# Optimization experiments

Measured on AMD Instinct MI355X. Metric: run time of the kernel, lower is better.

Reference implementation:

```python
import jax, jax.numpy as jnp
import numpy as np

N = 50000        # nodes
E = 800000       # edges (avg degree 16)
F_IN = 128
H = 128
C = 16


def setup_inputs() -> dict:
    key = jax.random.key(0)
    ks = jax.random.split(key, 12)
    x = jax.random.normal(ks[0], (N, F_IN), dtype=jnp.float32)
    edges = jax.random.randint(ks[1], (2, E), 0, N, dtype=jnp.int32)
    dims = [(F_IN, H), (H, H // 2), (H // 2, H // 4), (H // 4, H // 8), (H // 8, C)]
    params = {}
    for i, (di, do) in enumerate(dims):
        params[f"W{i+1}"] = jax.random.normal(ks[2 + 2 * i], (di, do), dtype=jnp.float32) * (1.0 / np.sqrt(di)).astype(np.float32)
        params[f"b{i+1}"] = jax.random.normal(ks[3 + 2 * i], (do,), dtype=jnp.float32) * 0.01
    return {"x": x, "edges": edges, **params}


def reference(x, edges, W1, b1, W2, b2, W3, b3, W4, b4, W5, b5):
    src, dst = edges[0], edges[1]
    ones = jnp.ones((E,), x.dtype)
    # symmetric ('both') normalization with degree clamped to >= 1 (DGL GraphConv default)
    out_deg = jnp.clip(jax.ops.segment_sum(ones, src, num_segments=N), 1.0, None)
    in_deg = jnp.clip(jax.ops.segment_sum(ones, dst, num_segments=N), 1.0, None)
    norm_src = (out_deg ** -0.5)[:, None]   # [N,1]
    norm_dst = (in_deg ** -0.5)[:, None]    # [N,1]

    def graph_conv(h, W, b):
        h = h @ W                                  # dense transform first (out <= in)
        msgs = (h * norm_src)[src]                 # [E, d_out] gather
        agg = jax.ops.segment_sum(msgs, dst, num_segments=N)  # scatter-add SpMM
        return agg * norm_dst + b

    h = x
    for W, b in ((W1, b1), (W2, b2), (W3, b3), (W4, b4), (W5, b5)):
        h = jax.nn.relu(graph_conv(h, W, b))
    return h
```

## Files before the change

### kernel.cpp

```cpp
#include <hip/hip_runtime.h>
#include <hip/hip_bf16.h>


#define THREADS 256
#define HIST_B 128
#define HWORDS 12500
#define RS_BLOCKS 196
#define G1BLKS 782
#define C4 (HIST_B / 4)

typedef __attribute__((ext_vector_type(8))) short short8_t;
typedef __attribute__((ext_vector_type(4))) float float4_t;

__device__ __forceinline__ unsigned short f2bf_rne(float f) {
    unsigned u = __builtin_bit_cast(unsigned, f);
    unsigned r = u + 0x7fffu + ((u >> 16) & 1u);
    return (unsigned short)(r >> 16);
}
__device__ __forceinline__ float bf2f(unsigned short h) {
    return __builtin_bit_cast(float, ((unsigned)h) << 16);
}

template<int NT, bool NORM, bool ASCALE>
__device__ __forceinline__ void quant_epilogue(float4_t* acc, const float* __restrict__ norm,
                                               const float* __restrict__ ascale,
                                               short* __restrict__ outq, float* __restrict__ qscale,
                                               int M, int blk, int tid,
                                               int ostride, int ocol0, int qstride, int qoff) {
    const int w    = tid >> 6;
    const int lane = tid & 63;
    const int ln   = lane & 15;
    const int quad = lane >> 4;
    const int orow = blk * 64 + w * 16 + quad * 4;
#pragma unroll
    for (int i = 0; i < 4; ++i) {
        int r = orow + i;
        float m = 0.f;
#pragma unroll
        for (int nt = 0; nt < NT; ++nt) m = fmaxf(m, fabsf(acc[nt][i]));
#pragma unroll
        for (int off = 1; off < 16; off <<= 1) m = fmaxf(m, __shfl_xor(m, off));
        float s = 1.f;
        if (NORM) s = (r < M) ? norm[r] : 0.f;
        if (ASCALE && r < M) s *= ascale[r];
        float rowmax = m * s;
        float inv = (rowmax > 0.f) ? (32767.f / rowmax) : 0.f;
        if (r < M) {
            if (ln == 0) qscale[r * qstride + qoff] = rowmax * (1.f / 32767.f);
#pragma unroll
            for (int nt = 0; nt < NT; ++nt)
                outq[(size_t)r * ostride + ocol0 + nt * 16 + ln] =
                    (short)(int)__builtin_rintf(acc[nt][i] * s * inv);
        }
    }
}

template<int K, int NOUT>
__device__ __forceinline__ void gemm_core_q(const short* __restrict__ Aq,
                                            const float* __restrict__ ascale,
                                            const short* lh, const short* ll,
                                            const float* __restrict__ norm,
                                            short* __restrict__ outq, float* __restrict__ qscale,
                                            int M, int blk, int tid) {
    constexpr int Kp  = (K + 31) & ~31;
    constexpr int STR = Kp + 8;
    constexpr int NT  = NOUT / 16;
    const int w    = tid >> 6;
    const int lane = tid & 63;
    const int ln   = lane & 15;
    const int quad = lane >> 4;
    const int row  = blk * 64 + w * 16 + ln;
    const bool rv  = row < M;

    float4_t acc[NT];
#pragma unroll
    for (int i = 0; i < NT; ++i) acc[i] = (float4_t){0.f, 0.f, 0.f, 0.f};

#pragma unroll
    for (int kt = 0; kt < Kp / 32; ++kt) {
        const int k0 = kt * 32 + quad * 8;
        short8_t qv = (short8_t)(short)0;
        if (rv && k0 < K) qv = *(const short8_t*)&Aq[(size_t)row * K + k0];
        short8_t ahi, alo;
#pragma unroll
        for (int j = 0; j < 8; ++j) {
            float a = (float)qv[j];
            unsigned short h = f2bf_rne(a);
            ahi[j] = (short)h;
            alo[j] = (short)f2bf_rne(a - bf2f(h));
        }
#pragma unroll
        for (int nt = 0; nt < NT; ++nt) {
            const int bidx = (nt * 16 + ln) * STR + kt * 32 + quad * 8;
            short8_t bh = *(const short8_t*)&lh[bidx];
            short8_t bl = *(const short8_t*)&ll[bidx];
            acc[nt] = __builtin_amdgcn_mfma_f32_16x16x32_bf16(ahi, bh, acc[nt], 0, 0, 0);
            acc[nt] = __builtin_amdgcn_mfma_f32_16x16x32_bf16(ahi, bl, acc[nt], 0, 0, 0);
            acc[nt] = __builtin_amdgcn_mfma_f32_16x16x32_bf16(alo, bh, acc[nt], 0, 0, 0);
        }
    }
    quant_epilogue<NT, true, true>(acc, norm, ascale, outq, qscale, M, blk, tid,
                                   NOUT, 0, 1, 0);
}

template<int K, int NOUT, int DINP>
__device__ __forceinline__ void gemm_core_lds(const float* As,
                                              const short* lh, const short* ll,
                                              const float* __restrict__ norm,
                                              short* __restrict__ outq, float* __restrict__ qscale,
                                              int M, int blk, int tid) {
    constexpr int Kp  = (K + 31) & ~31;
    constexpr int STR = Kp + 8;
    constexpr int NT  = NOUT / 16;
    const int w    = tid >> 6;
    const int lane = tid & 63;
    const int ln   = lane & 15;
    const int quad = lane >> 4;
    const int rloc = w * 16 + ln;
    const bool rv  = (blk * 64 + rloc) < M;

    float4_t acc[NT];
#pragma unroll
    for (int i = 0; i < NT; ++i) acc[i] = (float4_t){0.f, 0.f, 0.f, 0.f};

#pragma unroll
    for (int kt = 0; kt < Kp / 32; ++kt) {
        const int k0 = kt * 32 + quad * 8;
        float a[8];
        if (rv && k0 < K) {
            float4 v0 = *(const float4*)&As[rloc * DINP + k0];
            float4 v1 = *(const float4*)&As[rloc * DINP + k0 + 4];
            a[0] = v0.x; a[1] = v0.y; a[2] = v0.z; a[3] = v0.w;
            a[4] = v1.x; a[5] = v1.y; a[6] = v1.z; a[7] = v1.w;
        } else {
#pragma unroll
            for (int j = 0; j < 8; ++j) a[j] = 0.f;
        }
        short8_t ahi, alo;
#pragma unroll
        for (int j = 0; j < 8; ++j) {
            unsigned short h = f2bf_rne(a[j]);
            ahi[j] = (short)h;
            alo[j] = (short)f2bf_rne(a[j] - bf2f(h));
        }
#pragma unroll
        for (int nt = 0; nt < NT; ++nt) {
            const int bidx = (nt * 16 + ln) * STR + kt * 32 + quad * 8;
            short8_t bh = *(const short8_t*)&lh[bidx];
            short8_t bl = *(const short8_t*)&ll[bidx];
            acc[nt] = __builtin_amdgcn_mfma_f32_16x16x32_bf16(ahi, bh, acc[nt], 0, 0, 0);
            acc[nt] = __builtin_amdgcn_mfma_f32_16x16x32_bf16(ahi, bl, acc[nt], 0, 0, 0);
            acc[nt] = __builtin_amdgcn_mfma_f32_16x16x32_bf16(alo, bh, acc[nt], 0, 0, 0);
        }
    }
    quant_epilogue<NT, true, false>(acc, norm, nullptr, outq, qscale, M, blk, tid,
                                    NOUT, 0, 1, 0);
}

__device__ __forceinline__ void conv_one(const float* __restrict__ W, short* __restrict__ hi,
                                         short* __restrict__ lo, int K, int NOUT, int STR, int i) {
    int n = i / STR;
    int kk = i % STR;
    float v = (kk < K) ? W[(size_t)kk * NOUT + n] : 0.f;
    unsigned short h = f2bf_rne(v);
    hi[i] = (short)h;
    lo[i] = (short)f2bf_rne(v - bf2f(h));
}

__global__ __launch_bounds__(THREADS)
void packed0_kernel(const float* __restrict__ x, const float* __restrict__ W1,
                    const float* __restrict__ W2, const float* __restrict__ W3,
                    const float* __restrict__ W4, const float* __restrict__ W5,
                    short* __restrict__ tq, float* __restrict__ qscale2,
                    const int* __restrict__ src, const int* __restrict__ dst,
                    unsigned* __restrict__ p_src, unsigned* __restrict__ p_dst,
                    unsigned char* __restrict__ rank, int* __restrict__ flags,
                    short* w2h, short* w2l, short* w3h, short* w3l,
                    short* w4h, short* w4l, short* w5h, short* w5l,
                    int E, int chunk, int N) {
    __shared__ __align__(16) char smem[50048];
    const int blk = blockIdx.x;
    const int t = threadIdx.x;

    if (blk < G1BLKS) {
        short* lh = (short*)smem;
        short* ll = (short*)smem + 8704;

        const int lane = t & 63;
        const int ln   = lane & 15;
        const int quad = lane >> 4;
        const int row  = blk * 64 + (t >> 6) * 16 + ln;
        const bool rv  = row < N;

        short8_t ahi[4], alo[4];
#pragma unroll
        for (int kt = 0; kt < 4; ++kt) {
            const int k0 = kt * 32 + quad * 8;
            float a[8];
            if (rv) {
                float4 v0 = *(const float4*)&x[(size_t)row * 128 + k0];
                float4 v1 = *(const float4*)&x[(size_t)row * 128 + k0 + 4];
                a[0] = v0.x; a[1] = v0.y; a[2] = v0.z; a[3] = v0.w;
                a[4] = v1.x; a[5] = v1.y; a[6] = v1.z; a[7] = v1.w;
            } else {
#pragma unroll
                for (int j = 0; j < 8; ++j) a[j] = 0.f;
            }
#pragma unroll
            for (int j = 0; j < 8; ++j) {
                unsigned short h = f2bf_rne(a[j]);
                ahi[kt][j] = (short)h;
                alo[kt][j] = (short)f2bf_rne(a[j] - bf2f(h));
            }
        }

        for (int h = 0; h < 2; ++h) {
            for (int j = t; j < 128 * 64; j += THREADS) {
                int kk = j >> 6, n = j & 63;
                float v = W1[kk * 128 + h * 64 + n];
                unsigned short hh = f2bf_rne(v);
                lh[n * 136 + kk] = (short)hh;
                ll[n * 136 + kk] = (short)f2bf_rne(v - bf2f(hh));
            }
            __syncthreads();

            float4_t acc[4];
#pragma unroll
            for (int i = 0; i < 4; ++i) acc[i] = (float4_t){0.f, 0.f, 0.f, 0.f};
#pragma unroll
            for (int kt = 0; kt < 4; ++kt) {
#pragma unroll
                for (int nt = 0; nt < 4; ++nt) {
                    const int bidx = (nt * 16 + ln) * 136 + kt * 32 + quad * 8;
                    short8_t bh = *(const short8_t*)&lh[bidx];
                    short8_t bl = *(const short8_t*)&ll[bidx];
                    acc[nt] = __builtin_amdgcn_mfma_f32_16x16x32_bf16(ahi[kt], bh, acc[nt], 0, 0, 0);
                    acc[nt] = __builtin_amdgcn_mfma_f32_16x16x32_bf16(ahi[kt], bl, acc[nt], 0, 0, 0);
                    acc[nt] = __builtin_amdgcn_mfma_f32_16x16x32_bf16(alo[kt], bh, acc[nt], 0, 0, 0);
                }
            }
            quant_epilogue<4, false, false>(acc, nullptr, nullptr, tq, qscale2, N, blk, t,
                                            128, h * 64, 2, h);
            if (h == 0) __syncthreads();
        }
    } else if (blk < G1BLKS + 2 * HIST_B) {
        unsigned* bins = (unsigned*)smem;
        const int hb = blk - G1BLKS;
        const bool is_dst = hb < HIST_B;
        const int b = is_dst ? hb : hb - HIST_B;
        const int e0 = b * chunk;
        int e1 = e0 + chunk; if (e1 > E) e1 = E;
        const int* __restrict__ idx = is_dst ? dst : src;
        unsigned* __restrict__ pout = is_dst ? p_dst : p_src;

        for (int w = t; w < HWORDS; w += THREADS) bins[w] = 0;
        __syncthreads();
        for (int e = e0 + t; e < e1; e += THREADS) {
            int d = idx[e];
            unsigned sh = (unsigned)(d & 3) * 8u;
            unsigned old = atomicAdd(&bins[d >> 2], 1u << sh);
            if (is_dst) rank[e] = (unsigned char)((old >> sh) & 0xffu);
        }
        __syncthreads();
        for (int w = t; w < HWORDS; w += THREADS)
            pout[(size_t)b * HWORDS + w] = bins[w];
    } else {
        int cb = blk - G1BLKS - 2 * HIST_B;
        if (cb == 48) {
            flags[t] = 0;
            return;
        }
        int i = cb * THREADS + t;
        if (i < 8704)                        conv_one(W2, w2h, w2l, 128, 64, 136, i);
        else if ((i -= 8704) < 2304)         conv_one(W3, w3h, w3l, 64, 32, 72, i);
        else if ((i -= 2304) < 640)          conv_one(W4, w4h, w4l, 32, 16, 40, i);
        else { i -= 640;                     conv_one(W5, w5h, w5l, 16, 16, 40, i); }
    }
}

__global__ __launch_bounds__(THREADS)
void reduce_scan_kernel(const unsigned* __restrict__ p_src, unsigned* __restrict__ p_dst,
                        float* __restrict__ norm_src, float* __restrict__ norm_dst,
                        float* __restrict__ qscale2, int* __restrict__ row_ptr,
                        int* __restrict__ flags, int N) {
    __shared__ unsigned qd[4][64];
    __shared__ unsigned qs[4][64];
    __shared__ int sscan[64];
    __shared__ int bexcl_sh;
    const int t  = threadIdx.x;
    const int b  = blockIdx.x;
    const int q  = t >> 6;
    const int wl = t & 63;
    const int w  = b * 64 + wl;
    const bool wv = (w < HWORDS);

    unsigned vals[C4];
    unsigned dsum = 0, ssum = 0;
    if (wv) {
#pragma unroll
        for (int i = 0; i < C4; ++i) {
            int c = q * C4 + i;
            vals[i] = p_dst[(size_t)c * HWORDS + w];
            dsum += vals[i];
        }
#pragma unroll
        for (int i = 0; i < C4; ++i) {
            int c = q * C4 + i;
            ssum += p_src[(size_t)c * HWORDS + w];
        }
    }
    qd[q][wl] = dsum;
    qs[q][wl] = ssum;
    __syncthreads();

    unsigned off = 0, dfull = 0, sfull = 0;
#pragma unroll
    for (int qq = 0; qq < 4; ++qq) {
        unsigned v = qd[qq][wl];
        if (qq < q) off += v;
        dfull += v;
        sfull += qs[qq][wl];
    }

    if (wv) {
        unsigned run = off;
#pragma unroll
        for (int i = 0; i < C4; ++i) {
            int c = q * C4 + i;
            p_dst[(size_t)c * HWORDS + w] = run;
            run += vals[i];
        }
    }

    int d0 = 0, d1 = 0, d2 = 0, d3 = 0, wdeg = 0;
    if (q == 0) {
        d0 = (int)(dfull & 0xffu); d1 = (int)((dfull >> 8) & 0xffu);
        d2 = (int)((dfull >> 16) & 0xffu); d3 = (int)(dfull >> 24);
        wdeg = d0 + d1 + d2 + d3;
        if (wv) {
#pragma unroll
            for (int l = 0; l < 4; ++l) {
                int node = 4 * w + l;
                int dd = (l == 0) ? d0 : (l == 1) ? d1 : (l == 2) ? d2 : d3;
                int ds = (int)((sfull >> (8 * l)) & 0xffu);
                norm_dst[node] = rsqrtf((float)(dd < 1 ? 1 : dd));
                float ns = rsqrtf((float)(ds < 1 ? 1 : ds));
                norm_src[node] = ns;
                qscale2[2 * node]     *= ns;
                qscale2[2 * node + 1] *= ns;
            }
        }
        sscan[wl] = wv ? wdeg : 0;
    }
    __syncthreads();
    for (int o = 1; o < 64; o <<= 1) {
        int u = 0;
        if (t < 64 && t >= o) u = sscan[t - o];
        __syncthreads();
        if (t < 64) sscan[t] += u;
        __syncthreads();
    }
    const int btotal = sscan[63];

    if (t == 0) atomicExch(&flags[b], btotal + 1);
    if (t < 64) {
        int v = 0;
        for (int p = t; p < b; p += 64) {
            int f;
            do { f = atomicAdd(&flags[p], 0); } while (f == 0);
            v += f - 1;
        }
#pragma unroll
        for (int o = 1; o < 64; o <<= 1) v += __shfl_xor(v, o);
        if (t == 0) bexcl_sh = v;
    }
    __syncthreads();

    if (q == 0 && wv) {
        int pre = bexcl_sh + sscan[wl] - wdeg;
        int n0 = 4 * w;
        row_ptr[n0 + 0] = pre; pre += d0;
        row_ptr[n0 + 1] = pre; pre += d1;
        row_ptr[n0 + 2] = pre; pre += d2;
        row_ptr[n0 + 3] = pre;
    }
    if (b == RS_BLOCKS - 1 && t == 0) row_ptr[N] = bexcl_sh + btotal;
}

__global__ __launch_bounds__(THREADS)
void scatter_kernel(const int* __restrict__ src, const int* __restrict__ dst,
                    const unsigned char* __restrict__ rank,
                    const int* __restrict__ row_ptr, const unsigned* __restrict__ p_dst,
                    int* __restrict__ col, int E, int chunk) {
    const int bc  = blockIdx.x >> 2;
    const int sub = blockIdx.x & 3;
    const int qch = (chunk + 3) >> 2;
    const int e0 = bc * chunk;
    int e1 = e0 + chunk; if (e1 > E) e1 = E;
    int s = e0 + sub * qch;
    int send = s + qch; if (send > e1) send = e1;
    for (int e = s + threadIdx.x; e < send; e += THREADS) {
        int d = dst[e];
        unsigned sh = (unsigned)(d & 3) * 8u;
        unsigned pre = (p_dst[(size_t)bc * HWORDS + (d >> 2)] >> sh) & 0xffu;
        col[row_ptr[d] + (int)pre + (int)rank[e]] = src[e];
    }
}

__global__ __launch_bounds__(THREADS)
void agg1_q_kernel(const short* __restrict__ tq, const float* __restrict__ qscale2,
                   const int* __restrict__ row_ptr, const int* __restrict__ col,
                   const float* __restrict__ norm_dst, const float* __restrict__ bias,
                   short* __restrict__ outq, float* __restrict__ qs_out, int N) {
    const int tid  = threadIdx.x;
    const int ln   = tid & 15;
    const int ep   = (tid >> 4) & 3;
    const int g    = tid >> 6;
    const int node = blockIdx.x * 4 + g;
    if (node >= N) return;

    const int half = ln >> 3;
    const int beg = row_ptr[node];
    const int end = row_ptr[node + 1];

    float acc[8];
#pragma unroll
    for (int c = 0; c < 8; ++c) acc[c] = 0.f;

    int j = beg + ep;
    for (; j + 4 < end; j += 8) {
        int s0 = col[j];
        int s1 = col[j + 4];
        short8_t v0 = *(const short8_t*)&tq[(size_t)s0 * 128 + ln * 8];
        short8_t v1 = *(const short8_t*)&tq[(size_t)s1 * 128 + ln * 8];
        float c0 = qscale2[2 * s0 + half];
        float c1 = qscale2[2 * s1 + half];
#pragma unroll
        for (int c = 0; c < 8; ++c)
            acc[c] += (float)v0[c] * c0 + (float)v1[c] * c1;
    }
    if (j < end) {
        int s0 = col[j];
        short8_t v0 = *(const short8_t*)&tq[(size_t)s0 * 128 + ln * 8];
        float c0 = qscale2[2 * s0 + half];
#pragma unroll
        for (int c = 0; c < 8; ++c) acc[c] += (float)v0[c] * c0;
    }

#pragma unroll
    for (int c = 0; c < 8; ++c) {
        acc[c] += __shfl_xor(acc[c], 16);
        acc[c] += __shfl_xor(acc[c], 32);
    }

    float nd = norm_dst[node];
    float vals[8];
    float m = 0.f;
#pragma unroll
    for (int c = 0; c < 8; ++c) {
        vals[c] = fmaxf(acc[c] * nd + bias[ln * 8 + c], 0.f);
        m = fmaxf(m, vals[c]);
    }
#pragma unroll
    for (int off = 1; off < 16; off <<= 1) m = fmaxf(m, __shfl_xor(m, off));
    float inv = (m > 0.f) ? (32767.f / m) : 0.f;

    if (ep == 0) {
        short8_t q;
#pragma unroll
        for (int c = 0; c < 8; ++c) q[c] = (short)(int)__builtin_rintf(vals[c] * inv);
        *(short8_t*)&outq[(size_t)node * 128 + ln * 8] = q;
        if (ln == 0) qs_out[node] = m * (1.f / 32767.f);
    }
}

template<int K, int NOUT>
__global__ __launch_bounds__(THREADS)
void gemm_mfma_q_kernel(const short* __restrict__ Aq, const float* __restrict__ ascale,
                        const short* __restrict__ wt_hi, const short* __restrict__ wt_lo,
                        const float* __restrict__ norm,
                        short* __restrict__ outq, float* __restrict__ qscale, int M) {
    constexpr int Kp  = (K + 31) & ~31;
    constexpr int STR = Kp + 8;

    __shared__ short lh[NOUT * STR];
    __shared__ short ll[NOUT * STR];

    const int tid = threadIdx.x;
    {
        constexpr int CNT = NOUT * STR / 2;
        const int* gh = (const int*)wt_hi;
        const int* gl = (const int*)wt_lo;
        int* sh = (int*)lh;
        int* sl = (int*)ll;
        for (int i = tid; i < CNT; i += THREADS) { sh[i] = gh[i]; sl[i] = gl[i]; }
    }
    __syncthreads();
    gemm_core_q<K, NOUT>(Aq, ascale, lh, ll, norm, outq, qscale, M, blockIdx.x, tid);
}

template<int D>
__global__ __launch_bounds__(THREADS)
void agg_q_kernel(const short* __restrict__ tq, const float* __restrict__ qscale,
                  const int* __restrict__ row_ptr, const int* __restrict__ col,
                  const float* __restrict__ norm_dst, const float* __restrict__ bias,
                  float* __restrict__ out, int N) {
    constexpr int TPN = D / 8;
    constexpr int NPB = THREADS / TPN;
    const int tid  = threadIdx.x;
    const int ln   = tid % TPN;
    const int g    = tid / TPN;
    const int node = blockIdx.x * NPB + g;
    if (node >= N) return;

    const int beg = row_ptr[node];
    const int end = row_ptr[node + 1];

    float acc[8];
#pragma unroll
    for (int c = 0; c < 8; ++c) acc[c] = 0.f;

    int j = beg;
    for (; j + 3 < end; j += 4) {
        int s0 = col[j], s1 = col[j + 1], s2 = col[j + 2], s3 = col[j + 3];
        short8_t v0 = *(const short8_t*)&tq[(size_t)s0 * D + ln * 8];
        short8_t v1 = *(const short8_t*)&tq[(size_t)s1 * D + ln * 8];
        short8_t v2 = *(const short8_t*)&tq[(size_t)s2 * D + ln * 8];
        short8_t v3 = *(const short8_t*)&tq[(size_t)s3 * D + ln * 8];
        float c0 = qscale[s0], c1 = qscale[s1], c2 = qscale[s2], c3 = qscale[s3];
#pragma unroll
        for (int c = 0; c < 8; ++c)
            acc[c] += (float)v0[c] * c0 + (float)v1[c] * c1
                    + (float)v2[c] * c2 + (float)v3[c] * c3;
    }
    for (; j < end; ++j) {
        int s0 = col[j];
        short8_t v0 = *(const short8_t*)&tq[(size_t)s0 * D + ln * 8];
        float c0 = qscale[s0];
#pragma unroll
        for (int c = 0; c < 8; ++c) acc[c] += (float)v0[c] * c0;
    }

    float nd = norm_dst[node];
    float4 b0 = *(const float4*)&bias[ln * 8];
    float4 b1 = *(const float4*)&bias[ln * 8 + 4];
    float4 o0, o1;
    o0.x = fmaxf(acc[0] * nd + b0.x, 0.f);
    o0.y = fmaxf(acc[1] * nd + b0.y, 0.f);
    o0.z = fmaxf(acc[2] * nd + b0.z, 0.f);
    o0.w = fmaxf(acc[3] * nd + b0.w, 0.f);
    o1.x = fmaxf(acc[4] * nd + b1.x, 0.f);
    o1.y = fmaxf(acc[5] * nd + b1.y, 0.f);
    o1.z = fmaxf(acc[6] * nd + b1.z, 0.f);
    o1.w = fmaxf(acc[7] * nd + b1.w, 0.f);
    *(float4*)&out[(size_t)node * D + ln * 8] = o0;
    *(float4*)&out[(size_t)node * D + ln * 8 + 4] = o1;
}

template<int DIN, int NOUT>
__global__ __launch_bounds__(THREADS)
void fused_agg_gemm_kernel(const short* __restrict__ tq_in, const float* __restrict__ qs_in,
                           const int* __restrict__ row_ptr, const int* __restrict__ col,
                           const float* __restrict__ norm_dst, const float* __restrict__ bias,
                           const short* __restrict__ wt_hi, const short* __restrict__ wt_lo,
                           const float* __restrict__ norm_src,
                           short* __restrict__ tq_out, float* __restrict__ qs_out, int N) {
    constexpr int Kp   = (DIN + 31) & ~31;
    constexpr int STR  = Kp + 8;
    constexpr int DINP = DIN + 4;
    constexpr int TPN  = DIN / 8;

    __shared__ float As[64 * DINP];
    __shared__ short lh[NOUT * STR];
    __shared__ short ll[NOUT * STR];

    const int tid = threadIdx.x;
    {
        constexpr int CNT = NOUT * STR / 2;
        const int* gh = (const int*)wt_hi;
        const int* gl = (const int*)wt_lo;
        int* sh = (int*)lh;
        int* sl = (int*)ll;
        for (int i = tid; i < CNT; i += THREADS) { sh[i] = gh[i]; sl[i] = gl[i]; }
    }

    const int ln = tid % TPN;
    for (int n0 = tid / TPN; n0 < 64; n0 += THREADS / TPN) {
        const int node = blockIdx.x * 64 + n0;
        if (node < N) {
            const int beg = row_ptr[node];
            const int end = row_ptr[node + 1];
            float acc[8];
#pragma unroll
            for (int c = 0; c < 8; ++c) acc[c] = 0.f;
            int j = beg;
            for (; j + 3 < end; j += 4) {
                int s0 = col[j], s1 = col[j + 1], s2 = col[j + 2], s3 = col[j + 3];
                short8_t v0 = *(const short8_t*)&tq_in[(size_t)s0 * DIN + ln * 8];
                short8_t v1 = *(const short8_t*)&tq_in[(size_t)s1 * DIN + ln * 8];
                short8_t v2 = *(const short8_t*)&tq_in[(size_t)s2 * DIN + ln * 8];
                short8_t v3 = *(const short8_t*)&tq_in[(size_t)s3 * DIN + ln * 8];
                float c0 = qs_in[s0], c1 = qs_in[s1], c2 = qs_in[s2], c3 = qs_in[s3];
#pragma unroll
                for (int c = 0; c < 8; ++c)
                    acc[c] += (float)v0[c] * c0 + (float)v1[c] * c1
                            + (float)v2[c] * c2 + (float)v3[c] * c3;
            }
            for (; j < end; ++j) {
                int s0 = col[j];
                short8_t v0 = *(const short8_t*)&tq_in[(size_t)s0 * DIN + ln * 8];
                float c0 = qs_in[s0];
#pragma unroll
                for (int c = 0; c < 8; ++c) acc[c] += (float)v0[c] * c0;
            }
            float nd = norm_dst[node];
#pragma unroll
            for (int c = 0; c < 8; ++c)
                As[n0 * DINP + ln * 8 + c] = fmaxf(acc[c] * nd + bias[ln * 8 + c], 0.f);
        }
    }
    __syncthreads();

    gemm_core_lds<DIN, NOUT, DINP>(As, lh, ll, norm_src, tq_out, qs_out, N, blockIdx.x, tid);
}

extern "C" void kernel_launch(void* const* d_in, const int* in_sizes, int n_in,
                              void* d_out, int out_size, void* d_ws, size_t ws_size,
                              hipStream_t stream) {
    const float* x     = (const float*)d_in[0];
    const int*   edges = (const int*)d_in[1];
    const float* W1 = (const float*)d_in[2];  const float* b1 = (const float*)d_in[3];
    const float* W2 = (const float*)d_in[4];  const float* b2 = (const float*)d_in[5];
    const float* W3 = (const float*)d_in[6];  const float* b3 = (const float*)d_in[7];
    const float* W4 = (const float*)d_in[8];  const float* b4 = (const float*)d_in[9];
    const float* W5 = (const float*)d_in[10]; const float* b5 = (const float*)d_in[11];

    const int N = in_sizes[0] / 128;
    const int E = in_sizes[1] / 2;
    const int* src = edges;
    const int* dst = edges + E;

    char* ws = (char*)d_ws;
    size_t off = 0;
    auto carve = [&](size_t bytes) -> void* {
        void* p = ws + off;
        off += (bytes + 255) & ~(size_t)255;
        return p;
    };
    short* tqA      = (short*)carve((size_t)N * 128 * 2);
    short* tqB      = (short*)carve((size_t)N * 64 * 2);
    short* tqH      = (short*)carve((size_t)N * 128 * 2);
    float* norm_src = (float*)carve((size_t)N * 4);
    float* norm_dst = (float*)carve((size_t)N * 4);
    int*   row_ptr  = (int*)carve((size_t)(N + 1) * 4);
    int*   col      = (int*)carve((size_t)E * 4);
    float* qsA      = (float*)carve((size_t)2 * N * 4);
    float* qsB      = (float*)carve((size_t)N * 4);
    float* qsH      = (float*)carve((size_t)N * 4);
    int*   flags    = (int*)carve((size_t)256 * 4);
    short* wts      = (short*)carve((size_t)24576 * 2);
    unsigned* p_src = (unsigned*)carve((size_t)HIST_B * HWORDS * 4);
    unsigned* p_dst = (unsigned*)carve((size_t)HIST_B * HWORDS * 4);
    unsigned char* rank = (unsigned char*)carve((size_t)E);
    (void)ws_size;

    short* w2h = wts;            short* w2l = w2h + 8704;
    short* w3h = w2l + 8704;     short* w3l = w3h + 2304;
    short* w4h = w3l + 2304;     short* w4l = w4h + 640;
    short* w5h = w4l + 640;      short* w5l = w5h + 640;

    const int chunk = (E + HIST_B - 1) / HIST_B;
    const int gridG = (N + 63) / 64;

    packed0_kernel<<<G1BLKS + 2 * HIST_B + 49, THREADS, 0, stream>>>(
        x, W1, W2, W3, W4, W5, tqA, qsA, src, dst, p_src, p_dst, rank, flags,
        w2h, w2l, w3h, w3l, w4h, w4l, w5h, w5l, E, chunk, N);

    reduce_scan_kernel<<<RS_BLOCKS, THREADS, 0, stream>>>(
        p_src, p_dst, norm_src, norm_dst, qsA, row_ptr, flags, N);

    scatter_kernel<<<4 * HIST_B, THREADS, 0, stream>>>(src, dst, rank, row_ptr, p_dst, col, E, chunk);

    agg1_q_kernel<<<(N + 3) / 4, THREADS, 0, stream>>>(
        tqA, qsA, row_ptr, col, norm_dst, b1, tqH, qsH, N);

    gemm_mfma_q_kernel<128, 64><<<gridG, THREADS, 0, stream>>>(
        tqH, qsH, w2h, w2l, norm_src, tqA, qsA, N);

    fused_agg_gemm_kernel<64, 32><<<gridG, THREADS, 0, stream>>>(
        tqA, qsA, row_ptr, col, norm_dst, b2, w3h, w3l, norm_src, tqB, qsB, N);
    fused_agg_gemm_kernel<32, 16><<<gridG, THREADS, 0, stream>>>(
        tqB, qsB, row_ptr, col, norm_dst, b3, w4h, w4l, norm_src, tqA, qsA, N);
    fused_agg_gemm_kernel<16, 16><<<gridG, THREADS, 0, stream>>>(
        tqA, qsA, row_ptr, col, norm_dst, b4, w5h, w5l, norm_src, tqB, qsB, N);

    agg_q_kernel<16><<<(N + 127) / 128, THREADS, 0, stream>>>(
        tqB, qsB, row_ptr, col, norm_dst, b5, (float*)d_out, N);
}
```

Before: 260.0 us.

## Halve shared memory in fused first kernel via quarter-tiles and two-pass histograms

Cuts the packed0 kernel's shared-memory footprint from about 50KB to about 25KB so more blocks can be resident per CU. The first GEMM now processes W1 in four 32-column tiles instead of two 64-column tiles, which means four quantization scales per node instead of two, and the aggregation and scan kernels are updated to match. The degree histogram blocks now make two passes over their edge chunk, each covering half of the node range. The cost is twice the edge index reads and more block barriers in the histogram blocks, plus extra W1 staging rounds and scale traffic in the GEMM blocks.

```diff
diff --git a/kernel.cpp b/kernel.cpp
--- a/kernel.cpp
+++ b/kernel.cpp
@@ -5,6 +5,8 @@
 #define THREADS 256
 #define HIST_B 128
 #define HWORDS 12500
+#define HWORDS2 6250
+#define NPR 25000
 #define RS_BLOCKS 196
 #define G1BLKS 782
 #define C4 (HIST_B / 4)
@@ -171,20 +173,20 @@
 void packed0_kernel(const float* __restrict__ x, const float* __restrict__ W1,
                     const float* __restrict__ W2, const float* __restrict__ W3,
                     const float* __restrict__ W4, const float* __restrict__ W5,
-                    short* __restrict__ tq, float* __restrict__ qscale2,
+                    short* __restrict__ tq, float* __restrict__ qscale4,
                     const int* __restrict__ src, const int* __restrict__ dst,
                     unsigned* __restrict__ p_src, unsigned* __restrict__ p_dst,
                     unsigned char* __restrict__ rank, int* __restrict__ flags,
                     short* w2h, short* w2l, short* w3h, short* w3l,
                     short* w4h, short* w4l, short* w5h, short* w5l,
                     int E, int chunk, int N) {
-    __shared__ __align__(16) char smem[50048];
+    __shared__ __align__(16) char smem[25088];
     const int blk = blockIdx.x;
     const int t = threadIdx.x;
 
     if (blk < G1BLKS) {
         short* lh = (short*)smem;
-        short* ll = (short*)smem + 8704;
+        short* ll = (short*)smem + 4352;
 
         const int lane = t & 63;
         const int ln   = lane & 15;
@@ -214,23 +216,23 @@
             }
         }
 
-        for (int h = 0; h < 2; ++h) {
-            for (int j = t; j < 128 * 64; j += THREADS) {
-                int kk = j >> 6, n = j & 63;
-                float v = W1[kk * 128 + h * 64 + n];
+        for (int qt = 0; qt < 4; ++qt) {
+            for (int j = t; j < 128 * 32; j += THREADS) {
+                int kk = j >> 5, n = j & 31;
+                float v = W1[kk * 128 + qt * 32 + n];
                 unsigned short hh = f2bf_rne(v);
                 lh[n * 136 + kk] = (short)hh;
                 ll[n * 136 + kk] = (short)f2bf_rne(v - bf2f(hh));
             }
             __syncthreads();
 
-            float4_t acc[4];
-#pragma unroll
-            for (int i = 0; i < 4; ++i) acc[i] = (float4_t){0.f, 0.f, 0.f, 0.f};
+            float4_t acc[2];
+            acc[0] = (float4_t){0.f, 0.f, 0.f, 0.f};
+            acc[1] = (float4_t){0.f, 0.f, 0.f, 0.f};
 #pragma unroll
             for (int kt = 0; kt < 4; ++kt) {
 #pragma unroll
-                for (int nt = 0; nt < 4; ++nt) {
+                for (int nt = 0; nt < 2; ++nt) {
                     const int bidx = (nt * 16 + ln) * 136 + kt * 32 + quad * 8;
                     short8_t bh = *(const short8_t*)&lh[bidx];
                     short8_t bl = *(const short8_t*)&ll[bidx];
@@ -239,9 +241,9 @@
                     acc[nt] = __builtin_amdgcn_mfma_f32_16x16x32_bf16(alo[kt], bh, acc[nt], 0, 0, 0);
                 }
             }
-            quant_epilogue<4, false, false>(acc, nullptr, nullptr, tq, qscale2, N, blk, t,
-                                            128, h * 64, 2, h);
-            if (h == 0) __syncthreads();
+            quant_epilogue<2, false, false>(acc, nullptr, nullptr, tq, qscale4, N, blk, t,
+                                            128, qt * 32, 4, qt);
+            if (qt < 3) __syncthreads();
         }
     } else if (blk < G1BLKS + 2 * HIST_B) {
         unsigned* bins = (unsigned*)smem;
@@ -253,17 +255,24 @@
         const int* __restrict__ idx = is_dst ? dst : src;
         unsigned* __restrict__ pout = is_dst ? p_dst : p_src;
 
-        for (int w = t; w < HWORDS; w += THREADS) bins[w] = 0;
-        __syncthreads();
-        for (int e = e0 + t; e < e1; e += THREADS) {
-            int d = idx[e];
-            unsigned sh = (unsigned)(d & 3) * 8u;
-            unsigned old = atomicAdd(&bins[d >> 2], 1u << sh);
-            if (is_dst) rank[e] = (unsigned char)((old >> sh) & 0xffu);
-        }
-        __syncthreads();
-        for (int w = t; w < HWORDS; w += THREADS)
-            pout[(size_t)b * HWORDS + w] = bins[w];
+        for (int r = 0; r < 2; ++r) {
+            const int lo = r * NPR;
+            for (int w = t; w < HWORDS2; w += THREADS) bins[w] = 0;
+            __syncthreads();
+            for (int e = e0 + t; e < e1; e += THREADS) {
+                int d = idx[e];
+                int dl = d - lo;
+                if ((unsigned)dl < (unsigned)NPR) {
+                    unsigned sh = (unsigned)(dl & 3) * 8u;
+                    unsigned old = atomicAdd(&bins[dl >> 2], 1u << sh);
+                    if (is_dst) rank[e] = (unsigned char)((old >> sh) & 0xffu);
+                }
+            }
+            __syncthreads();
+            for (int w = t; w < HWORDS2; w += THREADS)
+                pout[(size_t)b * HWORDS + r * HWORDS2 + w] = bins[w];
+            if (r == 0) __syncthreads();
+        }
     } else {
         int cb = blk - G1BLKS - 2 * HIST_B;
         if (cb == 48) {
@@ -281,7 +290,7 @@
 __global__ __launch_bounds__(THREADS)
 void reduce_scan_kernel(const unsigned* __restrict__ p_src, unsigned* __restrict__ p_dst,
                         float* __restrict__ norm_src, float* __restrict__ norm_dst,
-                        float* __restrict__ qscale2, int* __restrict__ row_ptr,
+                        float* __restrict__ qscale4, int* __restrict__ row_ptr,
                         int* __restrict__ flags, int N) {
     __shared__ unsigned qd[4][64];
     __shared__ unsigned qs[4][64];
@@ -346,8 +355,10 @@
                 norm_dst[node] = rsqrtf((float)(dd < 1 ? 1 : dd));
                 float ns = rsqrtf((float)(ds < 1 ? 1 : ds));
                 norm_src[node] = ns;
-                qscale2[2 * node]     *= ns;
-                qscale2[2 * node + 1] *= ns;
+                qscale4[4 * node]     *= ns;
+                qscale4[4 * node + 1] *= ns;
+                qscale4[4 * node + 2] *= ns;
+                qscale4[4 * node + 3] *= ns;
             }
         }
         sscan[wl] = wv ? wdeg : 0;
@@ -408,7 +419,7 @@
 }
 
 __global__ __launch_bounds__(THREADS)
-void agg1_q_kernel(const short* __restrict__ tq, const float* __restrict__ qscale2,
+void agg1_q_kernel(const short* __restrict__ tq, const float* __restrict__ qscale4,
                    const int* __restrict__ row_ptr, const int* __restrict__ col,
                    const float* __restrict__ norm_dst, const float* __restrict__ bias,
                    short* __restrict__ outq, float* __restrict__ qs_out, int N) {
@@ -419,7 +430,7 @@
     const int node = blockIdx.x * 4 + g;
     if (node >= N) return;
 
-    const int half = ln >> 3;
+    const int qtr = ln >> 2;
     const int beg = row_ptr[node];
     const int end = row_ptr[node + 1];
 
@@ -433,8 +444,8 @@
         int s1 = col[j + 4];
         short8_t v0 = *(const short8_t*)&tq[(size_t)s0 * 128 + ln * 8];
         short8_t v1 = *(const short8_t*)&tq[(size_t)s1 * 128 + ln * 8];
-        float c0 = qscale2[2 * s0 + half];
-        float c1 = qscale2[2 * s1 + half];
+        float c0 = qscale4[4 * s0 + qtr];
+        float c1 = qscale4[4 * s1 + qtr];
 #pragma unroll
         for (int c = 0; c < 8; ++c)
             acc[c] += (float)v0[c] * c0 + (float)v1[c] * c1;
@@ -442,7 +453,7 @@
     if (j < end) {
         int s0 = col[j];
         short8_t v0 = *(const short8_t*)&tq[(size_t)s0 * 128 + ln * 8];
-        float c0 = qscale2[2 * s0 + half];
+        float c0 = qscale4[4 * s0 + qtr];
 #pragma unroll
         for (int c = 0; c < 8; ++c) acc[c] += (float)v0[c] * c0;
     }
@@ -654,7 +665,7 @@
     float* norm_dst = (float*)carve((size_t)N * 4);
     int*   row_ptr  = (int*)carve((size_t)(N + 1) * 4);
     int*   col      = (int*)carve((size_t)E * 4);
-    float* qsA      = (float*)carve((size_t)2 * N * 4);
+    float* qsA      = (float*)carve((size_t)4 * N * 4);
     float* qsB      = (float*)carve((size_t)N * 4);
     float* qsH      = (float*)carve((size_t)N * 4);
     int*   flags    = (int*)carve((size_t)256 * 4);
```

Measured after the change: 262.2 us. No clear change (+0.9%).
